# Optimization experiments

Measured on AMD Instinct MI355X. Metric: run time of the kernel, lower is better.

## Reference

```python
import jax, jax.numpy as jnp
import numpy as np

DIM = 128
HEADS = 4
EPS = 1e-5


def setup_inputs() -> dict:
    key = jax.random.key(0)
    ks = jax.random.split(key, 14)
    B, N, C = 1, 256, DIM
    s = 1.0 / np.sqrt(C)
    inp = {
        'pair': jax.random.normal(ks[0], (B, N, N, C), dtype=jnp.float32),
        'Wq': jax.random.normal(ks[1], (C, C), dtype=jnp.float32) * s,
        'bq': jnp.zeros((C,), dtype=jnp.float32),
        'Wk': jax.random.normal(ks[2], (C, C), dtype=jnp.float32) * s,
        'bk': jnp.zeros((C,), dtype=jnp.float32),
        'Wv': jax.random.normal(ks[3], (C, C), dtype=jnp.float32) * s,
        'bv': jnp.zeros((C,), dtype=jnp.float32),
        'Wg': jax.random.normal(ks[4], (C, C), dtype=jnp.float32) * s,
        'bg': jnp.zeros((C,), dtype=jnp.float32),
        'Wo': jax.random.normal(ks[5], (C, C), dtype=jnp.float32) * s,
        'bo': jnp.zeros((C,), dtype=jnp.float32),
        'gamma': jnp.ones((C,), dtype=jnp.float32),
        'beta': jnp.zeros((C,), dtype=jnp.float32),
    }
    return inp


def _layernorm(x, gamma, beta):
    mu = jnp.mean(x, axis=-1, keepdims=True)
    var = jnp.mean(jnp.square(x - mu), axis=-1, keepdims=True)
    return (x - mu) * jax.lax.rsqrt(var + EPS) * gamma + beta


def reference(pair, Wq, bq, Wk, bk, Wv, bv, Wg, bg, Wo, bo, gamma, beta):
    B, N, _, C = pair.shape
    H = HEADS
    Ch = C // H
    scale = Ch ** (-0.5)
    # projections: nn.Linear is x @ W.T + b
    q = (pair @ Wq.T + bq).reshape(B, N, N, H, Ch)
    k = (pair @ Wk.T + bk).reshape(B, N, N, H, Ch)
    v = (pair @ Wv.T + bv).reshape(B, N, N, H, Ch)
    # per-row attention: logits [B,H,N(i),N(j),N(k)]
    attn = jnp.einsum('bijhc,bikhc->bhijk', q, k) * scale
    attn = jax.nn.softmax(attn, axis=-1)
    out = jnp.einsum('bhijk,bikhc->bijhc', attn, v).reshape(B, N, N, C)
    gate = jax.nn.sigmoid(pair @ Wg.T + bg)
    out = out * gate
    out = out @ Wo.T + bo
    return _layernorm(pair + out, gamma, beta)
```

## Files before the change

### kernel.cpp

```cpp
#include <hip/hip_runtime.h>
#include <hip/hip_bf16.h>

#define NN 256
#define CC 128
#define HH 4
#define CHD 32

typedef __attribute__((ext_vector_type(8))) short bf16x8;
typedef __attribute__((ext_vector_type(4))) short bf16x4;
typedef __attribute__((ext_vector_type(4))) float f32x4;

static __device__ __forceinline__ short f2bf(float f) {
  union { float f; unsigned u; } un; un.f = f;
  unsigned r = un.u + 0x7fff + ((un.u >> 16) & 1);
  return (short)(r >> 16);
}
static __device__ __forceinline__ float bf2f(short s) {
  union { unsigned u; float f; } un;
  un.u = ((unsigned)(unsigned short)s) << 16;
  return un.f;
}

__global__ void prep_kernel(const float* __restrict__ Wq, const float* __restrict__ Wk,
                            const float* __restrict__ Wv, const float* __restrict__ Wg,
                            const float* __restrict__ Wo, short* __restrict__ wpk)
{
  const int c = blockIdx.x * 256 + threadIdx.x;
  const int w = c >> 11;
  const int rem = c & 2047;
  const int t = rem >> 8;
  const int kc = (rem >> 6) & 3;
  const int lane = rem & 63;
  const float* W = (w == 0) ? Wq : (w == 1) ? Wk : (w == 2) ? Wv : (w == 3) ? Wg : Wo;
  const int row = t * 16 + (lane & 15);
  const int col = kc * 32 + (lane >> 4) * 8;
  const float* src = W + row * CC + col;
  bf16x8 b;
  #pragma unroll
  for (int j = 0; j < 8; ++j) b[j] = f2bf(src[j]);
  *(bf16x8*)(wpk + (size_t)c * 8) = b;
}

__global__ __launch_bounds__(256) void proj_kernel(
    const float* __restrict__ pair, const short* __restrict__ wpk,
    const float* __restrict__ bq, const float* __restrict__ bk,
    const float* __restrict__ bv, const float* __restrict__ bg,
    short* __restrict__ qo, short* __restrict__ ko,
    short* __restrict__ vo, short* __restrict__ go)
{
  const int wid  = threadIdx.x >> 6;
  const int lane = threadIdx.x & 63;
  const int g    = lane >> 4;
  const int t16  = lane & 15;

  const short* wsrc = wpk + (size_t)wid * 16384;
  bf16x8 wf[8][4];
  #pragma unroll
  for (int t = 0; t < 8; ++t)
    #pragma unroll
    for (int kc = 0; kc < 4; ++kc)
      wf[t][kc] = *(const bf16x8*)(wsrc + ((t*4 + kc)*64 + lane) * 8);

  const float* bias = (wid == 0) ? bq : (wid == 1) ? bk : (wid == 2) ? bv : bg;
  f32x4 bcol[8];
  #pragma unroll
  for (int t = 0; t < 8; ++t) bcol[t] = *(const f32x4*)(bias + t*16 + g*4);

  short* outp = (wid == 0) ? qo : (wid == 1) ? ko : (wid == 2) ? vo : go;
  const int row0 = blockIdx.x * 128;

  #pragma unroll 1
  for (int ch = 0; ch < 8; ++ch) {
    const int rbase = row0 + ch * 16;
    bf16x8 pf[4];
    #pragma unroll
    for (int kc = 0; kc < 4; ++kc) {
      const float* p = pair + (size_t)(rbase + t16) * CC + kc*32 + g*8;
      bf16x8 a;
      #pragma unroll
      for (int j = 0; j < 8; ++j) a[j] = f2bf(p[j]);
      pf[kc] = a;
    }
    f32x4 acc[8];
    #pragma unroll
    for (int t = 0; t < 8; ++t) acc[t] = f32x4{0.f, 0.f, 0.f, 0.f};
    #pragma unroll
    for (int kc = 0; kc < 4; ++kc)
      #pragma unroll
      for (int t = 0; t < 8; ++t)
        acc[t] = __builtin_amdgcn_mfma_f32_16x16x32_bf16(wf[t][kc], pf[kc], acc[t], 0, 0, 0);

    const size_t rowoff = (size_t)(rbase + t16) * CC;
    #pragma unroll
    for (int t = 0; t < 8; ++t) {
      f32x4 v;
      #pragma unroll
      for (int r = 0; r < 4; ++r) v[r] = acc[t][r] + bcol[t][r];
      if (wid == 3) {
        #pragma unroll
        for (int r = 0; r < 4; ++r) v[r] = 1.f / (1.f + __expf(-v[r]));
      }
      bf16x4 pk;
      #pragma unroll
      for (int r = 0; r < 4; ++r) pk[r] = f2bf(v[r]);
      *(bf16x4*)(outp + rowoff + t*16 + g*4) = pk;
    }
  }
}

__global__ __launch_bounds__(256) void attn_kernel(
    const short* __restrict__ qi, const short* __restrict__ ki,
    const short* __restrict__ vi, short* __restrict__ ao)
{
  __shared__ short Vt[32*264];
  __shared__ short Pl[4][16*264];

  const int bid  = blockIdx.x;
  const int i    = bid >> 2, h = bid & 3;
  const size_t pbase = (size_t)i * NN * CC + h * CHD;
  const int tid  = threadIdx.x;
  const int wid  = tid >> 6, lane = tid & 63;
  const int g    = lane >> 4, t16 = lane & 15;

  {
    const short* vr = vi + pbase + (size_t)tid * CC;
    #pragma unroll
    for (int u = 0; u < 4; ++u) {
      bf16x8 v8 = *(const bf16x8*)(vr + u*8);
      #pragma unroll
      for (int e = 0; e < 8; ++e)
        Vt[(u*8 + e)*264 + tid] = v8[e];
    }
  }
  __syncthreads();

  const float cs = 0.17677669529663689f * 1.4426950408889634f;

  #pragma unroll 1
  for (int c4 = 0; c4 < 4; ++c4) {
    const int q0 = wid*64 + c4*16;
    bf16x8 qf = *(const bf16x8*)(qi + pbase + (size_t)(q0 + t16)*CC + g*8);

    f32x4 s[16];
    #pragma unroll
    for (int t = 0; t < 16; ++t) {
      bf16x8 kf = *(const bf16x8*)(ki + pbase + (size_t)(t*16 + t16)*CC + g*8);
      s[t] = __builtin_amdgcn_mfma_f32_16x16x32_bf16(kf, qf, f32x4{0.f,0.f,0.f,0.f}, 0, 0, 0);
    }

    f32x4 m4 = s[0];
    #pragma unroll
    for (int t = 1; t < 16; ++t)
      #pragma unroll
      for (int r = 0; r < 4; ++r) m4[r] = fmaxf(m4[r], s[t][r]);
    float m = fmaxf(fmaxf(m4[0], m4[1]), fmaxf(m4[2], m4[3]));
    m = fmaxf(m, __shfl_xor(m, 16));
    m = fmaxf(m, __shfl_xor(m, 32));

    f32x4 s4 = f32x4{0.f,0.f,0.f,0.f};
    #pragma unroll
    for (int t = 0; t < 16; ++t) {
      f32x4 v = s[t];
      #pragma unroll
      for (int r = 0; r < 4; ++r) { v[r] = exp2f((v[r] - m) * cs); s4[r] += v[r]; }
      s[t] = v;
    }
    float sum = (s4[0] + s4[1]) + (s4[2] + s4[3]);
    sum += __shfl_xor(sum, 16);
    sum += __shfl_xor(sum, 32);
    const float sm = 1.f / sum;

    short* P = &Pl[wid][0];
    asm volatile("s_waitcnt lgkmcnt(0)" ::: "memory");
    #pragma unroll
    for (int t = 0; t < 16; ++t) {
      bf16x4 pk;
      #pragma unroll
      for (int r = 0; r < 4; ++r) pk[r] = f2bf(s[t][r]);
      *(bf16x4*)&P[t16*264 + t*16 + g*4] = pk;
    }
    asm volatile("s_waitcnt lgkmcnt(0)" ::: "memory");

    bf16x8 pa[8];
    #pragma unroll
    for (int kc = 0; kc < 8; ++kc)
      pa[kc] = *(const bf16x8*)&P[t16*264 + kc*32 + g*8];

    f32x4 o0 = f32x4{0.f,0.f,0.f,0.f};
    f32x4 o1 = f32x4{0.f,0.f,0.f,0.f};
    #pragma unroll
    for (int kc = 0; kc < 8; ++kc) {
      bf16x8 v0 = *(const bf16x8*)&Vt[t16*264 + kc*32 + g*8];
      bf16x8 v1 = *(const bf16x8*)&Vt[(16 + t16)*264 + kc*32 + g*8];
      o0 = __builtin_amdgcn_mfma_f32_16x16x32_bf16(v0, pa[kc], o0, 0, 0, 0);
      o1 = __builtin_amdgcn_mfma_f32_16x16x32_bf16(v1, pa[kc], o1, 0, 0, 0);
    }

    const size_t orow = pbase + (size_t)(q0 + t16) * CC;
    bf16x4 pk0, pk1;
    #pragma unroll
    for (int r = 0; r < 4; ++r) {
      pk0[r] = f2bf(o0[r] * sm);
      pk1[r] = f2bf(o1[r] * sm);
    }
    *(bf16x4*)(ao + orow + g*4)      = pk0;
    *(bf16x4*)(ao + orow + 16 + g*4) = pk1;
  }
}

__global__ __launch_bounds__(256) void out_kernel(
    const short* __restrict__ ai, const short* __restrict__ gi,
    const short* __restrict__ wpk_o, const float* __restrict__ bo,
    const float* __restrict__ pair, const float* __restrict__ gamma,
    const float* __restrict__ beta, float* __restrict__ out)
{
  __shared__ short Wl[16384];
  const int tid = threadIdx.x;
  const int wid = tid >> 6, lane = tid & 63;
  const int g = lane >> 4, t16 = lane & 15;

  #pragma unroll
  for (int it = 0; it < 8; ++it) {
    const int c = it*256 + tid;
    *(bf16x8*)&Wl[c*8] = *(const bf16x8*)(wpk_o + (size_t)c*8);
  }
  __syncthreads();

  const int m0 = blockIdx.x*64 + wid*16;
  const size_t rowoff = (size_t)(m0 + t16) * CC;

  bf16x8 xf[4];
  #pragma unroll
  for (int kc = 0; kc < 4; ++kc) {
    bf16x8 a8 = *(const bf16x8*)(ai + rowoff + kc*32 + g*8);
    bf16x8 g8 = *(const bf16x8*)(gi + rowoff + kc*32 + g*8);
    bf16x8 o;
    #pragma unroll
    for (int j = 0; j < 8; ++j) o[j] = f2bf(bf2f(a8[j]) * bf2f(g8[j]));
    xf[kc] = o;
  }

  f32x4 acc[8];
  #pragma unroll
  for (int t = 0; t < 8; ++t) acc[t] = f32x4{0.f,0.f,0.f,0.f};
  #pragma unroll
  for (int kc = 0; kc < 4; ++kc)
    #pragma unroll
    for (int t = 0; t < 8; ++t) {
      bf16x8 wfr = *(const bf16x8*)&Wl[((t*4 + kc)*64 + lane)*8];
      acc[t] = __builtin_amdgcn_mfma_f32_16x16x32_bf16(wfr, xf[kc], acc[t], 0, 0, 0);
    }

  float val[8][4];
  #pragma unroll
  for (int t = 0; t < 8; ++t) {
    f32x4 b4 = *(const f32x4*)(bo + t*16 + g*4);
    f32x4 p4 = *(const f32x4*)(pair + rowoff + t*16 + g*4);
    #pragma unroll
    for (int r = 0; r < 4; ++r) val[t][r] = acc[t][r] + b4[r] + p4[r];
  }
  float sum = 0.f;
  #pragma unroll
  for (int t = 0; t < 8; ++t)
    #pragma unroll
    for (int r = 0; r < 4; ++r) sum += val[t][r];
  sum += __shfl_xor(sum, 16); sum += __shfl_xor(sum, 32);
  const float mu = sum * (1.f/128.f);
  float sq = 0.f;
  #pragma unroll
  for (int t = 0; t < 8; ++t)
    #pragma unroll
    for (int r = 0; r < 4; ++r) { float d = val[t][r] - mu; sq += d*d; }
  sq += __shfl_xor(sq, 16); sq += __shfl_xor(sq, 32);
  const float rstd = rsqrtf(sq * (1.f/128.f) + 1e-5f);

  #pragma unroll
  for (int t = 0; t < 8; ++t) {
    f32x4 g4 = *(const f32x4*)(gamma + t*16 + g*4);
    f32x4 b4 = *(const f32x4*)(beta  + t*16 + g*4);
    f32x4 o4;
    #pragma unroll
    for (int r = 0; r < 4; ++r) o4[r] = (val[t][r] - mu) * rstd * g4[r] + b4[r];
    *(f32x4*)(out + rowoff + t*16 + g*4) = o4;
  }
}

extern "C" void kernel_launch(void* const* d_in, const int* in_sizes, int n_in,
                              void* d_out, int out_size, void* d_ws, size_t ws_size,
                              hipStream_t stream) {
  const float* pair  = (const float*)d_in[0];
  const float* Wq    = (const float*)d_in[1];
  const float* bq    = (const float*)d_in[2];
  const float* Wk    = (const float*)d_in[3];
  const float* bk    = (const float*)d_in[4];
  const float* Wv    = (const float*)d_in[5];
  const float* bv    = (const float*)d_in[6];
  const float* Wg    = (const float*)d_in[7];
  const float* bg    = (const float*)d_in[8];
  const float* Wo    = (const float*)d_in[9];
  const float* bo    = (const float*)d_in[10];
  const float* gamma = (const float*)d_in[11];
  const float* beta  = (const float*)d_in[12];
  float* out = (float*)d_out;

  short* wpk  = (short*)d_ws;
  short* q_ws = wpk + 81920;
  short* k_ws = q_ws + 8388608;
  short* v_ws = k_ws + 8388608;
  short* g_ws = v_ws + 8388608;
  short* a_ws = v_ws;

  hipLaunchKernelGGL(prep_kernel, dim3(40), dim3(256), 0, stream,
                     Wq, Wk, Wv, Wg, Wo, wpk);
  hipLaunchKernelGGL(proj_kernel, dim3(512), dim3(256), 0, stream,
                     pair, wpk, bq, bk, bv, bg, q_ws, k_ws, v_ws, g_ws);
  hipLaunchKernelGGL(attn_kernel, dim3(1024), dim3(256), 0, stream,
                     q_ws, k_ws, v_ws, a_ws);
  hipLaunchKernelGGL(out_kernel, dim3(1024), dim3(256), 0, stream,
                     a_ws, g_ws, wpk + 4*16384, bo, pair, gamma, beta, out);
}
```

Baseline: 208.0 us.

## Prefetch pair rows in projection, swizzle attention LDS, hoist out-kernel loads

The projection kernel now handles 64 rows per block across twice as many blocks, with launch bounds targeting two blocks per CU. It loads each next 16-row chunk of pair as float4 vectors while the current chunk is in MFMA, a register double-buffer meant to hide global load latency. The attention kernel replaces padded LDS arrays with XOR-swizzled layouts and processes P in two halves, which cuts LDS footprint and bank conflicts. The output kernel issues its attention and gate loads before staging the weights, so they overlap that copy. The attention output buffer now aliases q instead of v. All of this adds register pressure, and the aliasing change has to hold up when blocks overwrite q rows that other blocks may still read.

```diff
diff --git a/kernel.cpp b/kernel.cpp
--- a/kernel.cpp
+++ b/kernel.cpp
@@ -3,8 +3,6 @@
 
 #define NN 256
 #define CC 128
-#define HH 4
-#define CHD 32
 
 typedef __attribute__((ext_vector_type(8))) short bf16x8;
 typedef __attribute__((ext_vector_type(4))) short bf16x4;
@@ -28,11 +26,11 @@
   const int c = blockIdx.x * 256 + threadIdx.x;
   const int w = c >> 11;
   const int rem = c & 2047;
-  const int t = rem >> 8;
+  const int nt = rem >> 8;
   const int kc = (rem >> 6) & 3;
   const int lane = rem & 63;
   const float* W = (w == 0) ? Wq : (w == 1) ? Wk : (w == 2) ? Wv : (w == 3) ? Wg : Wo;
-  const int row = t * 16 + (lane & 15);
+  const int row = nt * 16 + (lane & 15);
   const int col = kc * 32 + (lane >> 4) * 8;
   const float* src = W + row * CC + col;
   bf16x8 b;
@@ -41,7 +39,7 @@
   *(bf16x8*)(wpk + (size_t)c * 8) = b;
 }
 
-__global__ __launch_bounds__(256) void proj_kernel(
+__global__ __launch_bounds__(256, 2) void proj_kernel(
     const float* __restrict__ pair, const short* __restrict__ wpk,
     const float* __restrict__ bq, const float* __restrict__ bk,
     const float* __restrict__ bv, const float* __restrict__ bg,
@@ -56,46 +54,66 @@
   const short* wsrc = wpk + (size_t)wid * 16384;
   bf16x8 wf[8][4];
   #pragma unroll
-  for (int t = 0; t < 8; ++t)
+  for (int nt = 0; nt < 8; ++nt)
     #pragma unroll
     for (int kc = 0; kc < 4; ++kc)
-      wf[t][kc] = *(const bf16x8*)(wsrc + ((t*4 + kc)*64 + lane) * 8);
+      wf[nt][kc] = *(const bf16x8*)(wsrc + ((nt*4 + kc)*64 + lane)*8);
 
   const float* bias = (wid == 0) ? bq : (wid == 1) ? bk : (wid == 2) ? bv : bg;
   f32x4 bcol[8];
   #pragma unroll
-  for (int t = 0; t < 8; ++t) bcol[t] = *(const f32x4*)(bias + t*16 + g*4);
+  for (int nt = 0; nt < 8; ++nt) bcol[nt] = *(const f32x4*)(bias + nt*16 + g*4);
 
   short* outp = (wid == 0) ? qo : (wid == 1) ? ko : (wid == 2) ? vo : go;
-  const int row0 = blockIdx.x * 128;
-
-  #pragma unroll 1
-  for (int ch = 0; ch < 8; ++ch) {
-    const int rbase = row0 + ch * 16;
+  const int row0 = blockIdx.x * 64;
+
+  f32x4 rawA[8];
+  {
+    const float* p0 = pair + (size_t)(row0 + t16) * CC + g*8;
+    #pragma unroll
+    for (int kc = 0; kc < 4; ++kc) {
+      rawA[kc*2]     = *(const f32x4*)(p0 + kc*32);
+      rawA[kc*2 + 1] = *(const f32x4*)(p0 + kc*32 + 4);
+    }
+  }
+
+  #pragma unroll
+  for (int mc = 0; mc < 4; ++mc) {
+    const int m = row0 + mc*16 + t16;
+    f32x4 rawB[8];
+    if (mc < 3) {
+      const float* pn = pair + (size_t)(m + 16) * CC + g*8;
+      #pragma unroll
+      for (int kc = 0; kc < 4; ++kc) {
+        rawB[kc*2]     = *(const f32x4*)(pn + kc*32);
+        rawB[kc*2 + 1] = *(const f32x4*)(pn + kc*32 + 4);
+      }
+    }
+
     bf16x8 pf[4];
     #pragma unroll
     for (int kc = 0; kc < 4; ++kc) {
-      const float* p = pair + (size_t)(rbase + t16) * CC + kc*32 + g*8;
       bf16x8 a;
       #pragma unroll
-      for (int j = 0; j < 8; ++j) a[j] = f2bf(p[j]);
+      for (int j = 0; j < 8; ++j) a[j] = f2bf(rawA[kc*2 + (j>>2)][j&3]);
       pf[kc] = a;
     }
+
     f32x4 acc[8];
     #pragma unroll
-    for (int t = 0; t < 8; ++t) acc[t] = f32x4{0.f, 0.f, 0.f, 0.f};
+    for (int nt = 0; nt < 8; ++nt) acc[nt] = f32x4{0.f,0.f,0.f,0.f};
     #pragma unroll
     for (int kc = 0; kc < 4; ++kc)
       #pragma unroll
-      for (int t = 0; t < 8; ++t)
-        acc[t] = __builtin_amdgcn_mfma_f32_16x16x32_bf16(wf[t][kc], pf[kc], acc[t], 0, 0, 0);
-
-    const size_t rowoff = (size_t)(rbase + t16) * CC;
-    #pragma unroll
-    for (int t = 0; t < 8; ++t) {
+      for (int nt = 0; nt < 8; ++nt)
+        acc[nt] = __builtin_amdgcn_mfma_f32_16x16x32_bf16(wf[nt][kc], pf[kc], acc[nt], 0, 0, 0);
+
+    const size_t rowoff = (size_t)m * CC;
+    #pragma unroll
+    for (int nt = 0; nt < 8; ++nt) {
       f32x4 v;
       #pragma unroll
-      for (int r = 0; r < 4; ++r) v[r] = acc[t][r] + bcol[t][r];
+      for (int r = 0; r < 4; ++r) v[r] = acc[nt][r] + bcol[nt][r];
       if (wid == 3) {
         #pragma unroll
         for (int r = 0; r < 4; ++r) v[r] = 1.f / (1.f + __expf(-v[r]));
@@ -103,7 +121,12 @@
       bf16x4 pk;
       #pragma unroll
       for (int r = 0; r < 4; ++r) pk[r] = f2bf(v[r]);
-      *(bf16x4*)(outp + rowoff + t*16 + g*4) = pk;
+      *(bf16x4*)(outp + rowoff + nt*16 + g*4) = pk;
+    }
+
+    if (mc < 3) {
+      #pragma unroll
+      for (int u = 0; u < 8; ++u) rawA[u] = rawB[u];
     }
   }
 }
@@ -112,39 +135,45 @@
     const short* __restrict__ qi, const short* __restrict__ ki,
     const short* __restrict__ vi, short* __restrict__ ao)
 {
-  __shared__ short Vt[32*264];
-  __shared__ short Pl[4][16*264];
+  __shared__ short Vsl[32*256];
+  __shared__ short Pl[4][2048];
 
   const int bid  = blockIdx.x;
   const int i    = bid >> 2, h = bid & 3;
-  const size_t pbase = (size_t)i * NN * CC + h * CHD;
   const int tid  = threadIdx.x;
   const int wid  = tid >> 6, lane = tid & 63;
   const int g    = lane >> 4, t16 = lane & 15;
+  const size_t mbase = (size_t)i * NN;
 
   {
-    const short* vr = vi + pbase + (size_t)tid * CC;
+    const short* vr = vi + (mbase + tid) * CC + h*32;
     #pragma unroll
     for (int u = 0; u < 4; ++u) {
       bf16x8 v8 = *(const bf16x8*)(vr + u*8);
       #pragma unroll
-      for (int e = 0; e < 8; ++e)
-        Vt[(u*8 + e)*264 + tid] = v8[e];
+      for (int e = 0; e < 8; ++e) {
+        const int ch = u*8 + e;
+        Vsl[ch*256 + (tid ^ ((ch & 7) << 3))] = v8[e];
+      }
     }
   }
   __syncthreads();
 
   const float cs = 0.17677669529663689f * 1.4426950408889634f;
+  const int swzP = (t16 & 7) << 3;
+  const int ch0 = t16, ch1 = 16 + t16;
+  const int swzV0 = (ch0 & 7) << 3, swzV1 = (ch1 & 7) << 3;
+  short* Pw = &Pl[wid][0];
 
   #pragma unroll 1
-  for (int c4 = 0; c4 < 4; ++c4) {
-    const int q0 = wid*64 + c4*16;
-    bf16x8 qf = *(const bf16x8*)(qi + pbase + (size_t)(q0 + t16)*CC + g*8);
+  for (int cc = 0; cc < 4; ++cc) {
+    const int q0 = wid*64 + cc*16;
+    bf16x8 qf = *(const bf16x8*)(qi + (mbase + q0 + t16)*CC + h*32 + g*8);
 
     f32x4 s[16];
     #pragma unroll
     for (int t = 0; t < 16; ++t) {
-      bf16x8 kf = *(const bf16x8*)(ki + pbase + (size_t)(t*16 + t16)*CC + g*8);
+      bf16x8 kf = *(const bf16x8*)(ki + (mbase + t*16 + t16)*CC + h*32 + g*8);
       s[t] = __builtin_amdgcn_mfma_f32_16x16x32_bf16(kf, qf, f32x4{0.f,0.f,0.f,0.f}, 0, 0, 0);
     }
 
@@ -153,16 +182,16 @@
     for (int t = 1; t < 16; ++t)
       #pragma unroll
       for (int r = 0; r < 4; ++r) m4[r] = fmaxf(m4[r], s[t][r]);
-    float m = fmaxf(fmaxf(m4[0], m4[1]), fmaxf(m4[2], m4[3]));
-    m = fmaxf(m, __shfl_xor(m, 16));
-    m = fmaxf(m, __shfl_xor(m, 32));
+    float mx = fmaxf(fmaxf(m4[0], m4[1]), fmaxf(m4[2], m4[3]));
+    mx = fmaxf(mx, __shfl_xor(mx, 16));
+    mx = fmaxf(mx, __shfl_xor(mx, 32));
 
     f32x4 s4 = f32x4{0.f,0.f,0.f,0.f};
     #pragma unroll
     for (int t = 0; t < 16; ++t) {
       f32x4 v = s[t];
       #pragma unroll
-      for (int r = 0; r < 4; ++r) { v[r] = exp2f((v[r] - m) * cs); s4[r] += v[r]; }
+      for (int r = 0; r < 4; ++r) { v[r] = exp2f((v[r] - mx) * cs); s4[r] += v[r]; }
       s[t] = v;
     }
     float sum = (s4[0] + s4[1]) + (s4[2] + s4[3]);
@@ -170,41 +199,42 @@
     sum += __shfl_xor(sum, 32);
     const float sm = 1.f / sum;
 
-    short* P = &Pl[wid][0];
-    asm volatile("s_waitcnt lgkmcnt(0)" ::: "memory");
-    #pragma unroll
-    for (int t = 0; t < 16; ++t) {
-      bf16x4 pk;
-      #pragma unroll
-      for (int r = 0; r < 4; ++r) pk[r] = f2bf(s[t][r]);
-      *(bf16x4*)&P[t16*264 + t*16 + g*4] = pk;
-    }
-    asm volatile("s_waitcnt lgkmcnt(0)" ::: "memory");
-
-    bf16x8 pa[8];
-    #pragma unroll
-    for (int kc = 0; kc < 8; ++kc)
-      pa[kc] = *(const bf16x8*)&P[t16*264 + kc*32 + g*8];
-
     f32x4 o0 = f32x4{0.f,0.f,0.f,0.f};
     f32x4 o1 = f32x4{0.f,0.f,0.f,0.f};
     #pragma unroll
-    for (int kc = 0; kc < 8; ++kc) {
-      bf16x8 v0 = *(const bf16x8*)&Vt[t16*264 + kc*32 + g*8];
-      bf16x8 v1 = *(const bf16x8*)&Vt[(16 + t16)*264 + kc*32 + g*8];
-      o0 = __builtin_amdgcn_mfma_f32_16x16x32_bf16(v0, pa[kc], o0, 0, 0, 0);
-      o1 = __builtin_amdgcn_mfma_f32_16x16x32_bf16(v1, pa[kc], o1, 0, 0, 0);
-    }
-
-    const size_t orow = pbase + (size_t)(q0 + t16) * CC;
+    for (int half = 0; half < 2; ++half) {
+      asm volatile("s_waitcnt lgkmcnt(0)" ::: "memory");
+      #pragma unroll
+      for (int tt = 0; tt < 8; ++tt) {
+        const int t = half*8 + tt;
+        bf16x4 pk;
+        #pragma unroll
+        for (int r = 0; r < 4; ++r) pk[r] = f2bf(s[t][r]);
+        *(bf16x4*)&Pw[t16*128 + ((tt*16 + g*4) ^ swzP)] = pk;
+      }
+      asm volatile("s_waitcnt lgkmcnt(0)" ::: "memory");
+
+      bf16x8 pa[4];
+      #pragma unroll
+      for (int kc = 0; kc < 4; ++kc)
+        pa[kc] = *(const bf16x8*)&Pw[t16*128 + ((kc*32 + g*8) ^ swzP)];
+
+      #pragma unroll
+      for (int kc = 0; kc < 4; ++kc) {
+        const int kb = half*128 + kc*32 + g*8;
+        bf16x8 v0 = *(const bf16x8*)&Vsl[ch0*256 + (kb ^ swzV0)];
+        bf16x8 v1 = *(const bf16x8*)&Vsl[ch1*256 + (kb ^ swzV1)];
+        o0 = __builtin_amdgcn_mfma_f32_16x16x32_bf16(v0, pa[kc], o0, 0, 0, 0);
+        o1 = __builtin_amdgcn_mfma_f32_16x16x32_bf16(v1, pa[kc], o1, 0, 0, 0);
+      }
+    }
+
+    const size_t ob = (mbase + q0 + t16)*CC + h*32;
     bf16x4 pk0, pk1;
     #pragma unroll
-    for (int r = 0; r < 4; ++r) {
-      pk0[r] = f2bf(o0[r] * sm);
-      pk1[r] = f2bf(o1[r] * sm);
-    }
-    *(bf16x4*)(ao + orow + g*4)      = pk0;
-    *(bf16x4*)(ao + orow + 16 + g*4) = pk1;
+    for (int r = 0; r < 4; ++r) { pk0[r] = f2bf(o0[r] * sm); pk1[r] = f2bf(o1[r] * sm); }
+    *(bf16x4*)(ao + ob + g*4)      = pk0;
+    *(bf16x4*)(ao + ob + 16 + g*4) = pk1;
   }
 }
 
@@ -219,6 +249,16 @@
   const int wid = tid >> 6, lane = tid & 63;
   const int g = lane >> 4, t16 = lane & 15;
 
+  const int m0 = blockIdx.x*64 + wid*16;
+  const size_t rowoff = (size_t)(m0 + t16) * CC;
+
+  bf16x8 a8[4], g8[4];
+  #pragma unroll
+  for (int kc = 0; kc < 4; ++kc) {
+    a8[kc] = *(const bf16x8*)(ai + rowoff + kc*32 + g*8);
+    g8[kc] = *(const bf16x8*)(gi + rowoff + kc*32 + g*8);
+  }
+
   #pragma unroll
   for (int it = 0; it < 8; ++it) {
     const int c = it*256 + tid;
@@ -226,62 +266,57 @@
   }
   __syncthreads();
 
-  const int m0 = blockIdx.x*64 + wid*16;
-  const size_t rowoff = (size_t)(m0 + t16) * CC;
-
   bf16x8 xf[4];
   #pragma unroll
   for (int kc = 0; kc < 4; ++kc) {
-    bf16x8 a8 = *(const bf16x8*)(ai + rowoff + kc*32 + g*8);
-    bf16x8 g8 = *(const bf16x8*)(gi + rowoff + kc*32 + g*8);
     bf16x8 o;
     #pragma unroll
-    for (int j = 0; j < 8; ++j) o[j] = f2bf(bf2f(a8[j]) * bf2f(g8[j]));
+    for (int j = 0; j < 8; ++j) o[j] = f2bf(bf2f(a8[kc][j]) * bf2f(g8[kc][j]));
     xf[kc] = o;
   }
 
   f32x4 acc[8];
   #pragma unroll
-  for (int t = 0; t < 8; ++t) acc[t] = f32x4{0.f,0.f,0.f,0.f};
+  for (int nt = 0; nt < 8; ++nt) acc[nt] = f32x4{0.f,0.f,0.f,0.f};
   #pragma unroll
   for (int kc = 0; kc < 4; ++kc)
     #pragma unroll
-    for (int t = 0; t < 8; ++t) {
-      bf16x8 wfr = *(const bf16x8*)&Wl[((t*4 + kc)*64 + lane)*8];
-      acc[t] = __builtin_amdgcn_mfma_f32_16x16x32_bf16(wfr, xf[kc], acc[t], 0, 0, 0);
+    for (int nt = 0; nt < 8; ++nt) {
+      bf16x8 wfr = *(const bf16x8*)&Wl[((nt*4 + kc)*64 + lane)*8];
+      acc[nt] = __builtin_amdgcn_mfma_f32_16x16x32_bf16(wfr, xf[kc], acc[nt], 0, 0, 0);
     }
 
   float val[8][4];
   #pragma unroll
-  for (int t = 0; t < 8; ++t) {
-    f32x4 b4 = *(const f32x4*)(bo + t*16 + g*4);
-    f32x4 p4 = *(const f32x4*)(pair + rowoff + t*16 + g*4);
-    #pragma unroll
-    for (int r = 0; r < 4; ++r) val[t][r] = acc[t][r] + b4[r] + p4[r];
+  for (int nt = 0; nt < 8; ++nt) {
+    f32x4 b4 = *(const f32x4*)(bo + nt*16 + g*4);
+    f32x4 p4 = *(const f32x4*)(pair + rowoff + nt*16 + g*4);
+    #pragma unroll
+    for (int r = 0; r < 4; ++r) val[nt][r] = acc[nt][r] + b4[r] + p4[r];
   }
   float sum = 0.f;
   #pragma unroll
-  for (int t = 0; t < 8; ++t)
-    #pragma unroll
-    for (int r = 0; r < 4; ++r) sum += val[t][r];
+  for (int nt = 0; nt < 8; ++nt)
+    #pragma unroll
+    for (int r = 0; r < 4; ++r) sum += val[nt][r];
   sum += __shfl_xor(sum, 16); sum += __shfl_xor(sum, 32);
   const float mu = sum * (1.f/128.f);
   float sq = 0.f;
   #pragma unroll
-  for (int t = 0; t < 8; ++t)
-    #pragma unroll
-    for (int r = 0; r < 4; ++r) { float d = val[t][r] - mu; sq += d*d; }
+  for (int nt = 0; nt < 8; ++nt)
+    #pragma unroll
+    for (int r = 0; r < 4; ++r) { float d = val[nt][r] - mu; sq += d*d; }
   sq += __shfl_xor(sq, 16); sq += __shfl_xor(sq, 32);
   const float rstd = rsqrtf(sq * (1.f/128.f) + 1e-5f);
 
   #pragma unroll
-  for (int t = 0; t < 8; ++t) {
-    f32x4 g4 = *(const f32x4*)(gamma + t*16 + g*4);
-    f32x4 b4 = *(const f32x4*)(beta  + t*16 + g*4);
+  for (int nt = 0; nt < 8; ++nt) {
+    f32x4 g4 = *(const f32x4*)(gamma + nt*16 + g*4);
+    f32x4 b4 = *(const f32x4*)(beta  + nt*16 + g*4);
     f32x4 o4;
     #pragma unroll
-    for (int r = 0; r < 4; ++r) o4[r] = (val[t][r] - mu) * rstd * g4[r] + b4[r];
-    *(f32x4*)(out + rowoff + t*16 + g*4) = o4;
+    for (int r = 0; r < 4; ++r) o4[r] = (val[nt][r] - mu) * rstd * g4[r] + b4[r];
+    *(f32x4*)(out + rowoff + nt*16 + g*4) = o4;
   }
 }
 
@@ -308,11 +343,11 @@
   short* k_ws = q_ws + 8388608;
   short* v_ws = k_ws + 8388608;
   short* g_ws = v_ws + 8388608;
-  short* a_ws = v_ws;
+  short* a_ws = q_ws;
 
   hipLaunchKernelGGL(prep_kernel, dim3(40), dim3(256), 0, stream,
                      Wq, Wk, Wv, Wg, Wo, wpk);
-  hipLaunchKernelGGL(proj_kernel, dim3(512), dim3(256), 0, stream,
+  hipLaunchKernelGGL(proj_kernel, dim3(1024), dim3(256), 0, stream,
                      pair, wpk, bq, bk, bv, bg, q_ws, k_ws, v_ws, g_ws);
   hipLaunchKernelGGL(attn_kernel, dim3(1024), dim3(256), 0, stream,
                      q_ws, k_ws, v_ws, a_ws);
```

After: 198.4 us. 4.6% less time.
